# Performance work log

Hardware: AMD Instinct MI355X
Metric: run time of the kernel (lower is better)

The kernel has to match this reference:

```python
import jax, jax.numpy as jnp
import numpy as np

T, N, FIN, HID, E = 3, 50000, 4, 128, 1600000
EPS = 1e-5


def setup_inputs() -> dict:
    key = jax.random.key(0)
    ks = jax.random.split(key, 16)
    s = 0.05
    return {
        "X": jax.random.normal(ks[0], (T, N, FIN), jnp.float32),
        "edge_index": jax.random.randint(ks[1], (2, E), 0, N, jnp.int64),
        "edge_weight": jax.random.uniform(ks[2], (E,), jnp.float32),
        "w1": jax.random.normal(ks[3], (FIN, HID), jnp.float32) * s,
        "wc": jax.random.normal(ks[4], (3, HID, HID), jnp.float32) * s,
        "bc": jnp.zeros((4, HID), jnp.float32),
        "bn_gamma": jnp.ones((4, HID), jnp.float32),
        "bn_beta": jnp.zeros((4, HID), jnp.float32),
        "lstm_wih": jax.random.normal(ks[5], (2, 4 * HID, HID), jnp.float32) * s,
        "lstm_whh": jax.random.normal(ks[6], (2, 4 * HID, HID), jnp.float32) * s,
        "lstm_b": jnp.zeros((2, 4 * HID), jnp.float32),
        "lin1_w": jax.random.normal(ks[7], (HID + T, HID), jnp.float32) * s,
        "lin1_b": jnp.zeros((HID,), jnp.float32),
        "lin2_w": jax.random.normal(ks[8], (HID, 1), jnp.float32) * s,
        "lin2_b": jnp.zeros((1,), jnp.float32),
    }


def reference(X, edge_index, edge_weight, w1, wc, bc, bn_gamma, bn_beta,
              lstm_wih, lstm_whh, lstm_b, lin1_w, lin1_b, lin2_w, lin2_b):
    n = X.shape[1]
    src, dst = edge_index[0], edge_index[1]
    loop = jnp.arange(n)
    # PyG gcn_norm: add self loops (weight 1), symmetric normalization
    src_a = jnp.concatenate([src, loop])
    dst_a = jnp.concatenate([dst, loop])
    w_a = jnp.concatenate([edge_weight, jnp.ones((n,), X.dtype)])
    deg = jax.ops.segment_sum(w_a, dst_a, num_segments=n)
    dinv = jnp.where(deg > 0, deg ** -0.5, 0.0)
    norm = dinv[src_a] * w_a * dinv[dst_a]  # [E+N]

    def gcn(x, w, b):
        h = x @ w                                   # [N,H] transform first (F small)
        msg = h[src_a] * norm[:, None]              # gather + scale
        return jax.ops.segment_sum(msg, dst_a, num_segments=n) + b

    def bn(h, g, beta):  # BatchNorm1d with batch stats (track_running_stats=False)
        mu = h.mean(0)
        var = ((h - mu) ** 2).mean(0)
        return (h - mu) / jnp.sqrt(var + EPS) * g + beta

    def per_timestep(x):
        h = bn(jax.nn.relu(gcn(x, w1, bc[0])), bn_gamma[0], bn_beta[0])
        for i in range(3):
            h = bn(jax.nn.relu(gcn(h, wc[i], bc[i + 1])), bn_gamma[i + 1], bn_beta[i + 1])
        return h

    C = jax.vmap(per_timestep)(X)  # [T, N, H]

    def lstm_layer(seq, wih, whh, b):
        hdim = whh.shape[1]
        h0 = jnp.zeros((seq.shape[1], hdim), seq.dtype)

        def step(carry, x):
            h, c = carry
            gates = x @ wih.T + h @ whh.T + b
            i, f, g, o = jnp.split(gates, 4, axis=-1)  # torch gate order i,f,g,o
            c = jax.nn.sigmoid(f) * c + jax.nn.sigmoid(i) * jnp.tanh(g)
            h = jax.nn.sigmoid(o) * jnp.tanh(c)
            return (h, c), h

        (hT, _), ys = jax.lax.scan(step, (h0, h0), seq)
        return ys, hT

    seq = C
    for layer in range(2):
        seq, hT = lstm_layer(seq, lstm_wih[layer], lstm_whh[layer], lstm_b[layer])

    h = jax.nn.relu(hT)                 # last layer's final hidden, [N, H]
    S = X[:, :, 0].T                    # [N, T]
    h = jnp.concatenate([h, S], axis=-1)
    h = h @ lin1_w + lin1_b
    h = h @ lin2_w + lin2_b             # dropout is identity at inference
    return h
```

## Files before the change

kernel.cpp:

```cpp
#include <hip/hip_runtime.h>
#include <hip/hip_fp8.h>
#include <cstdint>

#define TT  3
#define FIN 4
#define HID 128
#define RS16 384
#define RS32 192
#define RS8  384

typedef unsigned int   u32;
typedef unsigned short u16;
typedef unsigned char  u8;
typedef unsigned long long u64;
typedef float f32x2 __attribute__((ext_vector_type(2)));
typedef float f32x4 __attribute__((ext_vector_type(4)));
typedef __bf16 bf16x8 __attribute__((ext_vector_type(8)));

static __device__ __forceinline__ f32x4 mfma_bf16(bf16x8 a, bf16x8 b, f32x4 c) {
  return __builtin_amdgcn_mfma_f32_16x16x32_bf16(a, b, c, 0, 0, 0);
}
static __device__ __forceinline__ float sigf(float v) { return 1.f / (1.f + expf(-v)); }
static __device__ __forceinline__ float bf_lo(u32 u) { return __uint_as_float(u << 16); }
static __device__ __forceinline__ float bf_hi(u32 u) { return __uint_as_float(u & 0xffff0000u); }
static __device__ __forceinline__ u16 bfbits(float f) {
  return __builtin_bit_cast(unsigned short, (__bf16)f);
}
static __device__ __forceinline__ u8 f_to_fp8(float f) {
  __hip_fp8_e4m3 v(f); return (u8)v.__x;
}
static __device__ __forceinline__ f32x2 fp8x2_to_f32(u16 x) {
  return __builtin_amdgcn_cvt_pk_f32_fp8((int)(u32)x, false);
}


__global__ void k_init(u64* pk, float* stats, int* ticket, int n) {
  int i = blockIdx.x * 256 + threadIdx.x;
  if (i < n) pk[i] = 0ull;
  if (blockIdx.x == 0) {
    for (int k = 0; k < 3; ++k) stats[k * 256 + threadIdx.x] = 0.f;
    if (threadIdx.x == 0) *ticket = 0;
  }
}

__global__ void k_deg(const int* __restrict__ dstv, const float* __restrict__ ew,
                      u64* pk, int* __restrict__ epos, int E_) {
  int e = blockIdx.x * 256 + threadIdx.x;
  if (e < E_) {
    int d = dstv[e];
    u64 inc = (1ull << 42) | (u64)(ew[e] * 4294967296.0f);
    u64 old = atomicAdd(&pk[d], inc);
    epos[e] = (int)(old >> 42);
  }
}

__global__ __launch_bounds__(256) void k_scanA(const u64* __restrict__ pk, int* rowptr,
    int* partial, float* dinv, float* selfn, int n) {
  __shared__ int wsum[4];
  int tid = threadIdx.x, lane = tid & 63, wv = tid >> 6;
  int i = blockIdx.x * 256 + tid;
  int v = 0;
  if (i < n) {
    u64 p = pk[i];
    v = (int)(p >> 42);
    float degw = (float)((double)(p & ((1ull << 42) - 1)) * (1.0 / 4294967296.0) + 1.0);
    float r = rsqrtf(degw);
    dinv[i] = r; selfn[i] = r * r;
  }
  int inc = v;
  #pragma unroll
  for (int off = 1; off < 64; off <<= 1) {
    int t2 = __shfl_up(inc, off);
    if (lane >= off) inc += t2;
  }
  if (lane == 63) wsum[wv] = inc;
  __syncthreads();
  if (tid == 0) {
    int s = 0;
    #pragma unroll
    for (int j = 0; j < 4; ++j) { int t3 = wsum[j]; wsum[j] = s; s += t3; }
    partial[blockIdx.x] = s;
  }
  __syncthreads();
  int excl = wsum[wv] + inc - v;
  if (i <= n) rowptr[i] = excl;
}

__global__ __launch_bounds__(256) void k_scanB(int* partial, int nb) {
  __shared__ int wsum[4];
  int tid = threadIdx.x, lane = tid & 63, wv = tid >> 6;
  int v = (tid < nb) ? partial[tid] : 0;
  int inc = v;
  #pragma unroll
  for (int off = 1; off < 64; off <<= 1) {
    int t2 = __shfl_up(inc, off);
    if (lane >= off) inc += t2;
  }
  if (lane == 63) wsum[wv] = inc;
  __syncthreads();
  if (tid == 0) {
    int s = 0;
    #pragma unroll
    for (int j = 0; j < 4; ++j) { int t3 = wsum[j]; wsum[j] = s; s += t3; }
  }
  __syncthreads();
  int excl = wsum[wv] + inc - v;
  if (tid < nb) partial[tid] = excl;
}

__global__ void k_scanC(int* rowptr, const int* __restrict__ partial, int n) {
  int i = blockIdx.x * 256 + threadIdx.x;
  if (i <= n) rowptr[i] += partial[blockIdx.x];
}

__global__ void k_fillcsr(const int* __restrict__ srcv, const int* __restrict__ dstv,
                          const float* __restrict__ ew, const float* __restrict__ dinv,
                          const int* __restrict__ rowptr, const int* __restrict__ epos,
                          int2* __restrict__ csr, int E_) {
  int e = blockIdx.x * 256 + threadIdx.x;
  if (e < E_) {
    int d = dstv[e], s = srcv[e];
    int idx = rowptr[d] + epos[e];
    csr[idx] = make_int2(s, __float_as_int(dinv[s] * ew[e] * dinv[d]));
  }
}


__global__ __launch_bounds__(256) void k_aggX(const float* __restrict__ X,
    const int* __restrict__ rowptr, const int2* __restrict__ csr,
    const float* __restrict__ selfn, float* __restrict__ XA, int N_) {
  int wv = threadIdx.x >> 6, l = threadIdx.x & 63;
  int wid = blockIdx.x * 4 + wv, nw = gridDim.x * 4;
  for (int n = wid; n < N_; n += nw) {
    float acc[12];
    #pragma unroll
    for (int i = 0; i < 12; ++i) acc[i] = 0.f;
    int e0 = rowptr[n], e1 = rowptr[n + 1];
    for (int e = e0 + l; e < e1; e += 64) {
      int2 v2 = csr[e];
      int s = v2.x; float wn = __int_as_float(v2.y);
      #pragma unroll
      for (int t = 0; t < TT; ++t) {
        float4 v = *(const float4*)(X + ((size_t)t * N_ + s) * FIN);
        acc[t*4+0] += wn * v.x; acc[t*4+1] += wn * v.y;
        acc[t*4+2] += wn * v.z; acc[t*4+3] += wn * v.w;
      }
    }
    #pragma unroll
    for (int i = 0; i < 12; ++i)
      for (int off = 32; off; off >>= 1) acc[i] += __shfl_down(acc[i], off);
    if (l == 0) {
      float sn = selfn[n];
      #pragma unroll
      for (int t = 0; t < TT; ++t) {
        float4 v = *(const float4*)(X + ((size_t)t * N_ + n) * FIN);
        XA[(size_t)n*12 + t*4+0] = acc[t*4+0] + sn * v.x;
        XA[(size_t)n*12 + t*4+1] = acc[t*4+1] + sn * v.y;
        XA[(size_t)n*12 + t*4+2] = acc[t*4+2] + sn * v.z;
        XA[(size_t)n*12 + t*4+3] = acc[t*4+3] + sn * v.w;
      }
    }
  }
}

__global__ void k_l0c(const float* __restrict__ XA, const float* __restrict__ w1,
                      const float* __restrict__ bc0, u32* __restrict__ out32, int N_) {
  int tid = blockIdx.x * 256 + threadIdx.x;
  if (tid >= N_ * 64) return;
  int n = tid >> 6, l = tid & 63, cp = 2 * l;
  float w00 = w1[cp],       w01 = w1[cp+1];
  float w10 = w1[HID+cp],   w11 = w1[HID+cp+1];
  float w20 = w1[2*HID+cp], w21 = w1[2*HID+cp+1];
  float w30 = w1[3*HID+cp], w31 = w1[3*HID+cp+1];
  float b0 = bc0[cp], b1 = bc0[cp+1];
  const float* xa = XA + (size_t)n * 12;
  u32* orow = out32 + (size_t)n * RS32 + l;
  #pragma unroll
  for (int t = 0; t < TT; ++t) {
    float4 x = *(const float4*)(xa + t * 4);
    float v0 = fmaxf(b0 + x.x*w00 + x.y*w10 + x.z*w20 + x.w*w30, 0.f);
    float v1 = fmaxf(b1 + x.x*w01 + x.y*w11 + x.z*w21 + x.w*w31, 0.f);
    orow[t * 64] = (u32)bfbits(v0) | ((u32)bfbits(v1) << 16);
  }
}


__global__ __launch_bounds__(256) void k_stats3(const u32* __restrict__ H32, float* stats,
    int* ticket, const float* __restrict__ gamma, const float* __restrict__ beta,
    float* aff , int N_) {
  __shared__ float red[256][12];
  __shared__ int lastf;
  int l = threadIdx.x & 63, half = threadIdx.x >> 6;
  float s1[TT][2] = {}, s2[TT][2] = {};
  for (int n = blockIdx.x * 4 + half; n < N_; n += gridDim.x * 4) {
    const u32* row = H32 + (size_t)n * RS32 + l;
    #pragma unroll
    for (int t = 0; t < TT; ++t) {
      u32 u = row[t * 64];
      float v0 = bf_lo(u), v1 = bf_hi(u);
      s1[t][0] += v0; s2[t][0] += v0 * v0;
      s1[t][1] += v1; s2[t][1] += v1 * v1;
    }
  }
  #pragma unroll
  for (int t = 0; t < TT; ++t) {
    red[threadIdx.x][t*4+0] = s1[t][0]; red[threadIdx.x][t*4+1] = s2[t][0];
    red[threadIdx.x][t*4+2] = s1[t][1]; red[threadIdx.x][t*4+3] = s2[t][1];
  }
  __syncthreads();
  if (half == 0) {
    #pragma unroll
    for (int t = 0; t < TT; ++t) {
      float a0 = 0, a1 = 0, a2 = 0, a3 = 0;
      #pragma unroll
      for (int h2 = 0; h2 < 4; ++h2) {
        a0 += red[h2*64 + l][t*4+0]; a1 += red[h2*64 + l][t*4+1];
        a2 += red[h2*64 + l][t*4+2]; a3 += red[h2*64 + l][t*4+3];
      }
      atomicAdd(&stats[t*256 + 2*l], a0);       atomicAdd(&stats[t*256 + 128 + 2*l], a1);
      atomicAdd(&stats[t*256 + 2*l + 1], a2);   atomicAdd(&stats[t*256 + 128 + 2*l + 1], a3);
    }
  }
  __syncthreads();
  if (threadIdx.x == 0) {
    __threadfence();
    int tk = __hip_atomic_fetch_add(ticket, 1, __ATOMIC_ACQ_REL, __HIP_MEMORY_SCOPE_AGENT);
    lastf = (tk == (int)gridDim.x - 1) ? 1 : 0;
  }
  __syncthreads();
  if (lastf) {
    float invn = 1.f / (float)N_;
    for (int i = threadIdx.x; i < 384; i += 256) {
      int t = i >> 7, c = i & 127;
      float s1v = __hip_atomic_load(&stats[t*256 + c],       __ATOMIC_RELAXED, __HIP_MEMORY_SCOPE_AGENT);
      float s2v = __hip_atomic_load(&stats[t*256 + 128 + c], __ATOMIC_RELAXED, __HIP_MEMORY_SCOPE_AGENT);
      float mu = s1v * invn;
      float var = fmaxf(s2v * invn - mu * mu, 0.f);
      float a = gamma[c] * rsqrtf(var + 1e-5f);
      aff[t*256 + c] = a;
      aff[t*256 + 128 + c] = beta[c] - mu * a;
      stats[t*256 + c] = 0.f; stats[t*256 + 128 + c] = 0.f;
    }
    if (threadIdx.x == 0) *ticket = 0;
  }
}


__global__ void k_swzall(const float* __restrict__ wc, const float* __restrict__ wih,
                         const float* __restrict__ whh,
                         bf16x8* __restrict__ wcsw, bf16x8* __restrict__ wstk) {
  int id = blockIdx.x * 256 + threadIdx.x;
  if (id < 6144) {
    int i = id >> 11, lid = id & 2047;
    int l = lid & 63, frag = lid >> 6;
    int cb = frag & 7, kb = frag >> 3;
    int col = cb * 16 + (l & 15);
    int k0 = kb * 32 + (l >> 4) * 8;
    const float* W = wc + (size_t)i * HID * HID;
    bf16x8 v;
    #pragma unroll
    for (int j = 0; j < 8; ++j) v[j] = (__bf16)W[(size_t)(k0 + j) * HID + col];
    wcsw[i * 2048 + lid] = v;
  } else if (id < 6144 + 32768) {
    int id2 = id - 6144;
    int layer = id2 >> 14, lid = id2 & 16383;
    int l = lid & 63, frag = lid >> 6;
    int cb = frag & 31, kb = frag >> 5;
    int col = cb * 16 + (l & 15);
    int k0 = kb * 32 + (l >> 4) * 8;
    const float* wi = wih + (size_t)layer * 512 * HID;
    const float* wh = whh + (size_t)layer * 512 * HID;
    bf16x8 v;
    #pragma unroll
    for (int j = 0; j < 8; ++j) {
      int k = k0 + j;
      float val = (k < HID) ? wi[(size_t)col * HID + k] : wh[(size_t)col * HID + (k - HID)];
      v[j] = (__bf16)val;
    }
    wstk[layer * 16384 + lid] = v;
  }
}

__global__ void k_headprep(const float* __restrict__ l1w, const float* __restrict__ l1b,
                           const float* __restrict__ l2w, const float* __restrict__ l2b,
                           float* __restrict__ hw) {
  int k = threadIdx.x;
  if (k < HID + TT) {
    float s = 0.f;
    for (int j = 0; j < HID; ++j) s += l1w[(size_t)k * HID + j] * l2w[j];
    hw[k] = s;
  } else if (k == HID + TT) {
    float s = l2b[0];
    for (int j = 0; j < HID; ++j) s += l1b[j] * l2w[j];
    hw[HID + TT] = s;
  }
}


__global__ __launch_bounds__(256) void k_trans3(const u16* __restrict__ Xin,
    const float* __restrict__ aff, const bf16x8* __restrict__ wsw,
    u8* __restrict__ Y, int nblk, int N_) {
  int w = threadIdx.x >> 6, l = threadIdx.x & 63;
  int lr = l & 15, lk = l >> 4;
  int t = blockIdx.x / nblk;
  int blk = blockIdx.x - t * nblk;
  int rbase = blk * 64 + w * 16;
  int arow = rbase + lr;
  bool av = arow < N_;
  const float* fa = aff + t * 256;
  const float* fb = fa + 128;
  f32x4 acc[8];
  #pragma unroll
  for (int cb = 0; cb < 8; ++cb) acc[cb] = (f32x4){0.f, 0.f, 0.f, 0.f};
  #pragma unroll
  for (int kb = 0; kb < 4; ++kb) {
    int ko = kb * 32 + lk * 8;
    bf16x8 af;
    if (av) {
      uint4 u = *(const uint4*)(Xin + (size_t)arow * RS16 + t * 128 + ko);
      float4 a0 = *(const float4*)(fa + ko), a1 = *(const float4*)(fa + ko + 4);
      float4 b0 = *(const float4*)(fb + ko), b1 = *(const float4*)(fb + ko + 4);
      af[0] = (__bf16)(bf_lo(u.x) * a0.x + b0.x);
      af[1] = (__bf16)(bf_hi(u.x) * a0.y + b0.y);
      af[2] = (__bf16)(bf_lo(u.y) * a0.z + b0.z);
      af[3] = (__bf16)(bf_hi(u.y) * a0.w + b0.w);
      af[4] = (__bf16)(bf_lo(u.z) * a1.x + b1.x);
      af[5] = (__bf16)(bf_hi(u.z) * a1.y + b1.y);
      af[6] = (__bf16)(bf_lo(u.w) * a1.z + b1.z);
      af[7] = (__bf16)(bf_hi(u.w) * a1.w + b1.w);
    } else {
      #pragma unroll
      for (int j = 0; j < 8; ++j) af[j] = (__bf16)0.f;
    }
    #pragma unroll
    for (int cb = 0; cb < 8; ++cb) {
      bf16x8 bf = wsw[(kb * 8 + cb) * 64 + l];
      acc[cb] = mfma_bf16(af, bf, acc[cb]);
    }
  }
  #pragma unroll
  for (int cb = 0; cb < 8; ++cb)
    #pragma unroll
    for (int i2 = 0; i2 < 4; ++i2) {
      int orow = rbase + lk * 4 + i2;
      if (orow < N_)
        Y[(size_t)orow * RS8 + t * 128 + cb * 16 + lr] = f_to_fp8(acc[cb][i2]);
    }
}


__global__ __launch_bounds__(256) void k_agg3(const u8* __restrict__ H8,
    const int* __restrict__ rowptr, const int2* __restrict__ csr,
    const float* __restrict__ selfn, const float* __restrict__ bias,
    u16* __restrict__ outp, int N_) {
  int wv = threadIdx.x >> 6, l = threadIdx.x & 63;
  int wid = blockIdx.x * 4 + wv, nw = gridDim.x * 4;
  float b0 = bias[2 * l], b1 = bias[2 * l + 1];
  u32* O32 = (u32*)outp;
  for (int n = wid; n < N_; n += nw) {
    const u16* self = (const u16*)(H8 + (size_t)n * RS8) + l;
    float sn = selfn[n];
    f32x2 v0 = fp8x2_to_f32(self[0]);
    f32x2 v1 = fp8x2_to_f32(self[64]);
    f32x2 v2 = fp8x2_to_f32(self[128]);
    float a00 = sn * v0.x, a01 = sn * v0.y;
    float a10 = sn * v1.x, a11 = sn * v1.y;
    float a20 = sn * v2.x, a21 = sn * v2.y;
    int e0 = rowptr[n], e1 = rowptr[n + 1];
    int e = e0;
    for (; e + 3 < e1; e += 4) {
      int2 c0 = csr[e], c1 = csr[e+1], c2 = csr[e+2], c3 = csr[e+3];
      const u16* p0 = (const u16*)(H8 + (size_t)c0.x * RS8) + l;
      const u16* p1 = (const u16*)(H8 + (size_t)c1.x * RS8) + l;
      const u16* p2 = (const u16*)(H8 + (size_t)c2.x * RS8) + l;
      const u16* p3 = (const u16*)(H8 + (size_t)c3.x * RS8) + l;
      u16 x00 = p0[0], x01 = p0[64], x02 = p0[128];
      u16 x10 = p1[0], x11 = p1[64], x12 = p1[128];
      u16 x20 = p2[0], x21 = p2[64], x22 = p2[128];
      u16 x30 = p3[0], x31 = p3[64], x32 = p3[128];
      float w0 = __int_as_float(c0.y), w1v = __int_as_float(c1.y);
      float w2 = __int_as_float(c2.y), w3v = __int_as_float(c3.y);
      f32x2 y;
      y = fp8x2_to_f32(x00); a00 += w0 * y.x; a01 += w0 * y.y;
      y = fp8x2_to_f32(x10); a00 += w1v * y.x; a01 += w1v * y.y;
      y = fp8x2_to_f32(x20); a00 += w2 * y.x; a01 += w2 * y.y;
      y = fp8x2_to_f32(x30); a00 += w3v * y.x; a01 += w3v * y.y;
      y = fp8x2_to_f32(x01); a10 += w0 * y.x; a11 += w0 * y.y;
      y = fp8x2_to_f32(x11); a10 += w1v * y.x; a11 += w1v * y.y;
      y = fp8x2_to_f32(x21); a10 += w2 * y.x; a11 += w2 * y.y;
      y = fp8x2_to_f32(x31); a10 += w3v * y.x; a11 += w3v * y.y;
      y = fp8x2_to_f32(x02); a20 += w0 * y.x; a21 += w0 * y.y;
      y = fp8x2_to_f32(x12); a20 += w1v * y.x; a21 += w1v * y.y;
      y = fp8x2_to_f32(x22); a20 += w2 * y.x; a21 += w2 * y.y;
      y = fp8x2_to_f32(x32); a20 += w3v * y.x; a21 += w3v * y.y;
    }
    for (; e < e1; ++e) {
      int2 c0 = csr[e];
      const u16* p = (const u16*)(H8 + (size_t)c0.x * RS8) + l;
      float w = __int_as_float(c0.y);
      f32x2 y0 = fp8x2_to_f32(p[0]);
      f32x2 y1 = fp8x2_to_f32(p[64]);
      f32x2 y2 = fp8x2_to_f32(p[128]);
      a00 += w * y0.x; a01 += w * y0.y;
      a10 += w * y1.x; a11 += w * y1.y;
      a20 += w * y2.x; a21 += w * y2.y;
    }
    u32* orow = O32 + (size_t)n * RS32 + l;
    orow[0]   = (u32)bfbits(fmaxf(a00 + b0, 0.f)) | ((u32)bfbits(fmaxf(a01 + b1, 0.f)) << 16);
    orow[64]  = (u32)bfbits(fmaxf(a10 + b0, 0.f)) | ((u32)bfbits(fmaxf(a11 + b1, 0.f)) << 16);
    orow[128] = (u32)bfbits(fmaxf(a20 + b0, 0.f)) | ((u32)bfbits(fmaxf(a21 + b1, 0.f)) << 16);
  }
}


__global__ __launch_bounds__(256) void k_lstm(
    const u16* __restrict__ xb, int xs, const u16* __restrict__ hpb,
    const float* __restrict__ aff,
    float* __restrict__ cstate, u16* __restrict__ hout,
    const bf16x8* __restrict__ wsw, const float* __restrict__ bias,
    int first, int N_) {
  __shared__ __bf16 gl[32][512];
  int w = threadIdx.x >> 6, l = threadIdx.x & 63;
  int lr = l & 15, lk = l >> 4;
  int r0 = blockIdx.x * 32;
  f32x4 acc[2][8];
  #pragma unroll
  for (int rb = 0; rb < 2; ++rb)
    #pragma unroll
    for (int cb = 0; cb < 8; ++cb) acc[rb][cb] = (f32x4){0.f, 0.f, 0.f, 0.f};

  #pragma unroll
  for (int kb = 0; kb < 4; ++kb) {
    int ko = kb * 32 + lk * 8;
    bf16x8 af[2];
    #pragma unroll
    for (int rb = 0; rb < 2; ++rb) {
      int row = r0 + rb * 16 + lr;
      if (row < N_) {
        uint4 u = *(const uint4*)(xb + (size_t)row * xs + ko);
        if (aff) {
          float4 a0 = *(const float4*)(aff + ko),       a1 = *(const float4*)(aff + ko + 4);
          float4 b0 = *(const float4*)(aff + HID + ko), b1 = *(const float4*)(aff + HID + ko + 4);
          af[rb][0] = (__bf16)(bf_lo(u.x) * a0.x + b0.x);
          af[rb][1] = (__bf16)(bf_hi(u.x) * a0.y + b0.y);
          af[rb][2] = (__bf16)(bf_lo(u.y) * a0.z + b0.z);
          af[rb][3] = (__bf16)(bf_hi(u.y) * a0.w + b0.w);
          af[rb][4] = (__bf16)(bf_lo(u.z) * a1.x + b1.x);
          af[rb][5] = (__bf16)(bf_hi(u.z) * a1.y + b1.y);
          af[rb][6] = (__bf16)(bf_lo(u.w) * a1.z + b1.z);
          af[rb][7] = (__bf16)(bf_hi(u.w) * a1.w + b1.w);
        } else {
          af[rb] = __builtin_bit_cast(bf16x8, u);
        }
      } else {
        #pragma unroll
        for (int j = 0; j < 8; ++j) af[rb][j] = (__bf16)0.f;
      }
    }
    #pragma unroll
    for (int cb = 0; cb < 8; ++cb) {
      bf16x8 bf = wsw[(kb * 32 + w * 8 + cb) * 64 + l];
      acc[0][cb] = mfma_bf16(af[0], bf, acc[0][cb]);
      acc[1][cb] = mfma_bf16(af[1], bf, acc[1][cb]);
    }
  }
  if (!first) {
    #pragma unroll
    for (int kb = 0; kb < 4; ++kb) {
      int ko = kb * 32 + lk * 8;
      bf16x8 af[2];
      #pragma unroll
      for (int rb = 0; rb < 2; ++rb) {
        int row = r0 + rb * 16 + lr;
        if (row < N_) {
          af[rb] = __builtin_bit_cast(bf16x8, *(const uint4*)(hpb + (size_t)row * HID + ko));
        } else {
          #pragma unroll
          for (int j = 0; j < 8; ++j) af[rb][j] = (__bf16)0.f;
        }
      }
      #pragma unroll
      for (int cb = 0; cb < 8; ++cb) {
        bf16x8 bf = wsw[((kb + 4) * 32 + w * 8 + cb) * 64 + l];
        acc[0][cb] = mfma_bf16(af[0], bf, acc[0][cb]);
        acc[1][cb] = mfma_bf16(af[1], bf, acc[1][cb]);
      }
    }
  }
  #pragma unroll
  for (int rb = 0; rb < 2; ++rb)
    #pragma unroll
    for (int cb = 0; cb < 8; ++cb)
      #pragma unroll
      for (int i2 = 0; i2 < 4; ++i2)
        gl[rb * 16 + lk * 4 + i2][w * 128 + cb * 16 + lr] = (__bf16)acc[rb][cb][i2];
  __syncthreads();
  for (int it = threadIdx.x; it < 32 * HID; it += 256) {
    int nl = it >> 7, j = it & 127;
    int n = r0 + nl;
    if (n >= N_) continue;
    float ig = (float)gl[nl][j]       + bias[j];
    float fg = (float)gl[nl][128 + j] + bias[128 + j];
    float gg = (float)gl[nl][256 + j] + bias[256 + j];
    float og = (float)gl[nl][384 + j] + bias[384 + j];
    float cp = first ? 0.f : cstate[(size_t)n * HID + j];
    float cn = sigf(fg) * cp + sigf(ig) * tanhf(gg);
    float hn = sigf(og) * tanhf(cn);
    cstate[(size_t)n * HID + j] = cn;
    hout[(size_t)n * HID + j] = bfbits(hn);
  }
}


__global__ __launch_bounds__(256) void k_final2(const u32* __restrict__ H2,
    const float* __restrict__ Xin, const float* __restrict__ hw,
    float* __restrict__ outp, int N_) {
  int wv = threadIdx.x >> 6, l = threadIdx.x & 63;
  int wid = blockIdx.x * 4 + wv, nw = gridDim.x * 4;
  float wc0 = hw[2 * l], wc1 = hw[2 * l + 1];
  float ws0 = hw[HID], ws1 = hw[HID + 1], ws2 = hw[HID + 2], bb = hw[HID + 3];
  for (int n = wid; n < N_; n += nw) {
    u32 u = H2[(size_t)n * 64 + l];
    float p = fmaxf(bf_lo(u), 0.f) * wc0 + fmaxf(bf_hi(u), 0.f) * wc1;
    #pragma unroll
    for (int off = 32; off; off >>= 1) p += __shfl_down(p, off);
    if (l == 0) {
      p += Xin[(size_t)n * FIN] * ws0
         + Xin[((size_t)N_ + n) * FIN] * ws1
         + Xin[((size_t)2 * N_ + n) * FIN] * ws2;
      outp[n] = p + bb;
    }
  }
}


extern "C" void kernel_launch(void* const* d_in, const int* in_sizes, int n_in,
                              void* d_out, int out_size, void* d_ws, size_t ws_size,
                              hipStream_t stream) {
  const float* X   = (const float*)d_in[0];
  const int*   ei  = (const int*)  d_in[1];
  const float* ew  = (const float*)d_in[2];
  const float* w1  = (const float*)d_in[3];
  const float* wc  = (const float*)d_in[4];
  const float* bc  = (const float*)d_in[5];
  const float* gam = (const float*)d_in[6];
  const float* bet = (const float*)d_in[7];
  const float* wih = (const float*)d_in[8];
  const float* whh = (const float*)d_in[9];
  const float* lb  = (const float*)d_in[10];
  const float* l1w = (const float*)d_in[11];
  const float* l1b = (const float*)d_in[12];
  const float* l2w = (const float*)d_in[13];
  const float* l2b = (const float*)d_in[14];
  float* outp = (float*)d_out;
  (void)n_in; (void)out_size; (void)ws_size;

  const int N = in_sizes[0] / (TT * FIN);
  const int E = in_sizes[1] / 2;
  const int* srcv = ei;
  const int* dstv = ei + E;

  char* base = (char*)d_ws;
  size_t off = 0;
  auto alloc = [&](size_t b) -> void* {
    void* p = base + off;
    off += (b + 255) & ~(size_t)255;
    return p;
  };

  u64*   pk     = (u64*)  alloc((size_t)N * 8);
  int*   epos   = (int*)  alloc((size_t)E * 4);
  int*   rowptr = (int*)  alloc(((size_t)N + 1) * 4);
  int*   partial= (int*)  alloc(1024);
  float* dinv   = (float*)alloc((size_t)N * 4);
  float* selfn  = (float*)alloc((size_t)N * 4);
  int2*  csr    = (int2*) alloc((size_t)E * 8);
  float* XA     = (float*)alloc((size_t)N * 12 * 4);
  u16*   Ga     = (u16*)  alloc((size_t)N * RS16 * 2);
  u16*   Gb     = (u16*)  alloc((size_t)N * RS16 * 2);
  u8*    Htb    = (u8*)   alloc((size_t)N * RS8);
  u16*   Gcat   = (u16*)  alloc((size_t)N * RS16 * 2);
  float* stats  = (float*)alloc(768 * 4);
  int*   ticket = (int*)  alloc(256);
  float* affA   = (float*)alloc((size_t)3 * 256 * 4);
  float* aff3   = (float*)alloc((size_t)3 * 256 * 4);
  float* hw     = (float*)alloc(136 * 4);
  bf16x8* wcsw  = (bf16x8*)alloc((size_t)3 * 2048 * 16);
  bf16x8* wstk  = (bf16x8*)alloc((size_t)2 * 16384 * 16);
  u16*   Cb     = Ga;
  float* cbuf   = (float*)Gb;

  int gN = (N + 255) / 256, gE = (E + 255) / 256;
  int nb = (N + 255) / 256;
  int nblk = (N + 63) / 64;

  k_init<<<gN, 256, 0, stream>>>(pk, stats, ticket, N);
  k_deg<<<gE, 256, 0, stream>>>(dstv, ew, pk, epos, E);
  k_scanA<<<nb, 256, 0, stream>>>(pk, rowptr, partial, dinv, selfn, N);
  k_scanB<<<1, 256, 0, stream>>>(partial, nb);
  k_scanC<<<nb, 256, 0, stream>>>(rowptr, partial, N);
  k_fillcsr<<<gE, 256, 0, stream>>>(srcv, dstv, ew, dinv, rowptr, epos, csr, E);
  k_aggX<<<1024, 256, 0, stream>>>(X, rowptr, csr, selfn, XA, N);
  k_swzall<<<152, 256, 0, stream>>>(wc, wih, whh, wcsw, wstk);
  k_headprep<<<1, 256, 0, stream>>>(l1w, l1b, l2w, l2b, hw);

  k_l0c<<<(N * 64 + 255) / 256, 256, 0, stream>>>(XA, w1, bc, (u32*)Ga, N);
  k_stats3<<<256, 256, 0, stream>>>((const u32*)Ga, stats, ticket, gam, bet, affA, N);

  k_trans3<<<3 * nblk, 256, 0, stream>>>(Ga, affA, wcsw, Htb, nblk, N);
  k_agg3<<<2048, 256, 0, stream>>>(Htb, rowptr, csr, selfn, bc + HID, Gb, N);
  k_stats3<<<256, 256, 0, stream>>>((const u32*)Gb, stats, ticket, gam + HID, bet + HID, affA, N);

  k_trans3<<<3 * nblk, 256, 0, stream>>>(Gb, affA, wcsw + 2048, Htb, nblk, N);
  k_agg3<<<2048, 256, 0, stream>>>(Htb, rowptr, csr, selfn, bc + 2 * HID, Gb, N);
  k_stats3<<<256, 256, 0, stream>>>((const u32*)Gb, stats, ticket, gam + 2 * HID, bet + 2 * HID, affA, N);

  k_trans3<<<3 * nblk, 256, 0, stream>>>(Gb, affA, wcsw + 4096, Htb, nblk, N);
  k_agg3<<<2048, 256, 0, stream>>>(Htb, rowptr, csr, selfn, bc + 3 * HID, Gcat, N);
  k_stats3<<<256, 256, 0, stream>>>((const u32*)Gcat, stats, ticket, gam + 3 * HID, bet + 3 * HID, aff3, N);

  int gL = (N + 31) / 32;
  for (int t = 0; t < TT; ++t) {
    u16* Ct = Cb + (size_t)t * N * HID;
    const u16* hp = (t == 0) ? Ct : (Cb + (size_t)(t - 1) * N * HID);
    k_lstm<<<gL, 256, 0, stream>>>(Gcat + (size_t)t * HID, RS16, hp,
                                   aff3 + (size_t)t * 256, cbuf, Ct,
                                   wstk, lb, (t == 0) ? 1 : 0, N);
  }
  for (int t = 0; t < TT; ++t) {
    u16* Ct = Cb + (size_t)t * N * HID;
    const u16* hp = (t == 0) ? Ct : (Cb + (size_t)(t - 1) * N * HID);
    k_lstm<<<gL, 256, 0, stream>>>(Ct, HID, hp, nullptr, cbuf, Ct,
                                   wstk + 16384, lb + 512, (t == 0) ? 1 : 0, N);
  }
  k_final2<<<512, 256, 0, stream>>>((const u32*)(Cb + (size_t)2 * N * HID), X, hw, outp, N);
}
```

Before: 1.071 ms.

## Permute LSTM weight columns so each wave holds all four gates in registers

The stacked LSTM weights are reordered so that each wave's eight MFMA column blocks cover the i, f, g and o gates for the same 32 hidden units. The gate nonlinearity and cell update can then run directly on the accumulator registers, which removes the shared-memory staging buffer, the block barrier and the bf16 rounding of the gates. The bias is folded into the accumulator initialisation. The epilogue's global stores become strided, 16 lanes per row, which may coalesce less well than the old row-contiguous loop.

```diff
diff --git a/kernel.cpp b/kernel.cpp
--- a/kernel.cpp
+++ b/kernel.cpp
@@ -265,8 +265,8 @@
     int id2 = id - 6144;
     int layer = id2 >> 14, lid = id2 & 16383;
     int l = lid & 63, frag = lid >> 6;
-    int cb = frag & 31, kb = frag >> 5;
-    int col = cb * 16 + (l & 15);
+    int cb = frag & 7, q = (frag >> 3) & 3, kb = frag >> 5;
+    int col = (cb >> 1) * 128 + q * 32 + (cb & 1) * 16 + (l & 15);
     int k0 = kb * 32 + (l >> 4) * 8;
     const float* wi = wih + (size_t)layer * 512 * HID;
     const float* wh = whh + (size_t)layer * 512 * HID;
@@ -419,15 +419,16 @@
     float* __restrict__ cstate, u16* __restrict__ hout,
     const bf16x8* __restrict__ wsw, const float* __restrict__ bias,
     int first, int N_) {
-  __shared__ __bf16 gl[32][512];
-  int w = threadIdx.x >> 6, l = threadIdx.x & 63;
+  int l = threadIdx.x & 63, q = threadIdx.x >> 6;
   int lr = l & 15, lk = l >> 4;
   int r0 = blockIdx.x * 32;
   f32x4 acc[2][8];
   #pragma unroll
-  for (int rb = 0; rb < 2; ++rb)
-    #pragma unroll
-    for (int cb = 0; cb < 8; ++cb) acc[rb][cb] = (f32x4){0.f, 0.f, 0.f, 0.f};
+  for (int cb = 0; cb < 8; ++cb) {
+    float b = bias[(cb >> 1) * 128 + q * 32 + (cb & 1) * 16 + lr];
+    acc[0][cb] = (f32x4){b, b, b, b};
+    acc[1][cb] = acc[0][cb];
+  }
 
   #pragma unroll
   for (int kb = 0; kb < 4; ++kb) {
@@ -459,7 +460,7 @@
     }
     #pragma unroll
     for (int cb = 0; cb < 8; ++cb) {
-      bf16x8 bf = wsw[(kb * 32 + w * 8 + cb) * 64 + l];
+      bf16x8 bf = wsw[(size_t)(((kb * 4 + q) * 8 + cb) * 64 + l)];
       acc[0][cb] = mfma_bf16(af[0], bf, acc[0][cb]);
       acc[1][cb] = mfma_bf16(af[1], bf, acc[1][cb]);
     }
@@ -481,34 +482,33 @@
       }
       #pragma unroll
       for (int cb = 0; cb < 8; ++cb) {
-        bf16x8 bf = wsw[((kb + 4) * 32 + w * 8 + cb) * 64 + l];
+        bf16x8 bf = wsw[(size_t)((((kb + 4) * 4 + q) * 8 + cb) * 64 + l)];
         acc[0][cb] = mfma_bf16(af[0], bf, acc[0][cb]);
         acc[1][cb] = mfma_bf16(af[1], bf, acc[1][cb]);
       }
     }
   }
+
   #pragma unroll
   for (int rb = 0; rb < 2; ++rb)
     #pragma unroll
-    for (int cb = 0; cb < 8; ++cb)
+    for (int i2 = 0; i2 < 4; ++i2) {
+      int n = r0 + rb * 16 + lk * 4 + i2;
+      if (n >= N_) continue;
       #pragma unroll
-      for (int i2 = 0; i2 < 4; ++i2)
-        gl[rb * 16 + lk * 4 + i2][w * 128 + cb * 16 + lr] = (__bf16)acc[rb][cb][i2];
-  __syncthreads();
-  for (int it = threadIdx.x; it < 32 * HID; it += 256) {
-    int nl = it >> 7, j = it & 127;
-    int n = r0 + nl;
-    if (n >= N_) continue;
-    float ig = (float)gl[nl][j]       + bias[j];
-    float fg = (float)gl[nl][128 + j] + bias[128 + j];
-    float gg = (float)gl[nl][256 + j] + bias[256 + j];
-    float og = (float)gl[nl][384 + j] + bias[384 + j];
-    float cp = first ? 0.f : cstate[(size_t)n * HID + j];
-    float cn = sigf(fg) * cp + sigf(ig) * tanhf(gg);
-    float hn = sigf(og) * tanhf(cn);
-    cstate[(size_t)n * HID + j] = cn;
-    hout[(size_t)n * HID + j] = bfbits(hn);
-  }
+      for (int jb = 0; jb < 2; ++jb) {
+        int col = q * 32 + jb * 16 + lr;
+        float ig = acc[rb][jb][i2];
+        float fg = acc[rb][2 + jb][i2];
+        float gg = acc[rb][4 + jb][i2];
+        float og = acc[rb][6 + jb][i2];
+        float cp = first ? 0.f : cstate[(size_t)n * HID + col];
+        float cn = sigf(fg) * cp + sigf(ig) * tanhf(gg);
+        float hn = sigf(og) * tanhf(cn);
+        cstate[(size_t)n * HID + col] = cn;
+        hout[(size_t)n * HID + col] = bfbits(hn);
+      }
+    }
 }
 
 
```

Result: no change. 1.075 ms (+0.4%).
